# Performance work log

Measured on AMD Instinct MI355X. Metric: run time of the kernel, lower is better.

Reference implementation:

```python
import jax, jax.numpy as jnp
import numpy as np
from jax import lax

B, H, S = 256, 256, 512


def setup_inputs() -> dict:
    key = jax.random.key(0)
    ks = jax.random.split(key, 7)
    sc = 1.0 / np.sqrt(H).astype(np.float32)
    tree_state = jax.random.normal(ks[0], (B, H), jnp.float32)
    seq_states = jax.random.normal(ks[1], (B, H, S), jnp.float32)
    seq_mask = jax.random.randint(ks[2], (B, S), 0, 2, jnp.int32)
    W_ih = jax.random.uniform(ks[3], (3 * H, H), jnp.float32, -sc, sc)
    W_hh = jax.random.uniform(ks[4], (3 * H, H), jnp.float32, -sc, sc)
    b_ih = jax.random.uniform(ks[5], (3 * H,), jnp.float32, -sc, sc)
    b_hh = jax.random.uniform(ks[6], (3 * H,), jnp.float32, -sc, sc)
    return {"tree_state": tree_state, "seq_states": seq_states, "seq_mask": seq_mask,
            "W_ih": W_ih, "W_hh": W_hh, "b_ih": b_ih, "b_hh": b_hh}


def _gru_cell(x, h, W_ih, W_hh, b_ih, b_hh):
    # torch.nn.GRUCell math. x, h: (B, H); W_*: (3H, H); b_*: (3H,)
    gi = x @ W_ih.T + b_ih          # (B, 3H)
    gh = h @ W_hh.T + b_hh          # (B, 3H)
    i_r, i_z, i_n = jnp.split(gi, 3, axis=-1)
    h_r, h_z, h_n = jnp.split(gh, 3, axis=-1)
    r = jax.nn.sigmoid(i_r + h_r)
    z = jax.nn.sigmoid(i_z + h_z)
    n = jnp.tanh(i_n + r * h_n)
    return (1.0 - z) * n + z * h


def reference(tree_state, seq_states, seq_mask, W_ih, W_hh, b_ih, b_hh):
    # sequential recurrent scan over the seq axis of seq_states (batch, hid, seq)
    xs = jnp.transpose(seq_states, (2, 0, 1))  # (S, B, H)

    def step(h, x):
        h_new = _gru_cell(x, h, W_ih, W_hh, b_ih, b_hh)
        return h_new, h_new

    _, outs = lax.scan(step, tree_state, xs)      # (S, B, H)
    rnn_out = jnp.transpose(outs, (1, 0, 2))      # (B, S, H)
    # get_final_encoder_states: last unmasked timestep per row
    last_idx = jnp.maximum(jnp.sum(seq_mask, axis=1) - 1, 0)  # (B,)
    final = jnp.take_along_axis(rnn_out, last_idx[:, None, None], axis=1)  # (B,1,H)
    return final[:, 0, :]
```

## Files before the change

### kernel.cpp

```cpp
#include <hip/hip_runtime.h>
#include <hip/hip_bf16.h>

#define HH 256
#define SSL 512
#define G3 768

using short8 = __attribute__((ext_vector_type(8))) short;
using f32x4  = __attribute__((ext_vector_type(4))) float;

__device__ __forceinline__ unsigned short f2bf(float f) {
  unsigned int u = __float_as_uint(f);
  u += 0x7FFFu + ((u >> 16) & 1u);
  return (unsigned short)(u >> 16);
}
__device__ __forceinline__ float bf2f(unsigned short b) {
  return __uint_as_float(((unsigned int)b) << 16);
}
__device__ __forceinline__ void sync_step() {
  asm volatile("s_waitcnt lgkmcnt(0)" ::: "memory");
  __builtin_amdgcn_s_barrier();
  __builtin_amdgcn_sched_barrier(0);
}

__global__ __launch_bounds__(256) void prep_pack(
    const float* __restrict__ Wih, const float* __restrict__ Whh,
    unsigned short* __restrict__ wih_bf, unsigned short* __restrict__ whh_frag)
{
  int blk = blockIdx.x;
  if (blk < 96) {
    int base = (blk * 256 + threadIdx.x) * 4;
#pragma unroll
    for (int i = 0; i < 4; i++) {
      int u = base + i;
      float a = Wih[2 * u], b = Wih[2 * u + 1];
      ((unsigned int*)wih_bf)[u] = (unsigned int)f2bf(a) | ((unsigned int)f2bf(b) << 16);
    }
  } else {
    int gid = (blk - 96) * 256 + threadIdx.x;
    int f = gid >> 6, l = gid & 63;
    int kt = f & 7, mt = (f >> 3) & 3, g = (f >> 5) % 3, w = f / 96;
    int row = g * HH + w * 64 + mt * 16 + (l & 15);
    int k0  = kt * 32 + (l >> 4) * 8;
    const float* src = Whh + (size_t)row * HH + k0;
    unsigned int o[4];
#pragma unroll
    for (int i = 0; i < 4; i++)
      o[i] = (unsigned int)f2bf(src[2 * i]) | ((unsigned int)f2bf(src[2 * i + 1]) << 16);
    *(uint4*)(whh_frag + ((size_t)f * 64 + l) * 8) = *(uint4*)o;
  }
}

__global__ __launch_bounds__(512, 2) void gi_gemm(
    const float* __restrict__ X, const unsigned short* __restrict__ Wb,
    const float* __restrict__ bih, const float* __restrict__ bhh,
    unsigned short* __restrict__ gi)
{
  __shared__ __align__(16) unsigned short Al[128 * 256];
  __shared__ __align__(16) unsigned short Bl[128 * 256];
  __shared__ __align__(16) unsigned short Dl[64][136];
  __shared__ float biasl[G3];

  const int tid  = threadIdx.x;
  const int lane = tid & 63;
  const int wave = tid >> 6;
  const int wm   = wave >> 2;
  const int wn   = wave & 3;
  const int n16  = lane & 15;
  const int quad = lane >> 4;

  const int mblk = blockIdx.x;
  const int b    = mblk >> 2;
  const int s0   = (mblk & 3) * 128;

  const float* Xb = X + (size_t)b * (HH * SSL);

  for (int i = tid; i < G3; i += 512)
    biasl[i] = bih[i] + (i < 2 * HH ? bhh[i] : 0.f);

  float4 xs[4][2][2];
#pragma unroll
  for (int kt = 0; kt < 4; kt++)
#pragma unroll
    for (int q = 0; q < 2; q++) {
      int idx = tid + 512 * q, sq = idx & 31, a = idx >> 5;
      const float* p = Xb + (size_t)(kt * 64 + 2 * a) * SSL + s0 + 4 * sq;
      xs[kt][q][0] = *(const float4*)p;
      xs[kt][q][1] = *(const float4*)(p + SSL);
    }
#pragma unroll
  for (int kt = 0; kt < 4; kt++)
#pragma unroll
    for (int q = 0; q < 2; q++) {
      int idx = tid + 512 * q, sq = idx & 31, a = idx >> 5;
      int c = a >> 2, d = a & 3;
#pragma unroll
      for (int r = 0; r < 4; r++) {
        int s = 4 * sq + r;
        int sw = (s + (s >> 3)) & 7;
        unsigned int u =
            (unsigned int)f2bf(((const float*)&xs[kt][q][0])[r]) |
            ((unsigned int)f2bf(((const float*)&xs[kt][q][1])[r]) << 16);
        *(unsigned int*)(Al + s * 256 + kt * 64 + ((c ^ sw) * 8) + d * 2) = u;
      }
    }

  {
    uint4 wv[8];
#pragma unroll
    for (int p = 0; p < 8; p++) {
      int cid = tid + 512 * p, j = cid >> 5, c = cid & 31;
      wv[p] = *(const uint4*)(Wb + (size_t)(0 * 128 + j) * HH + c * 8);
    }
#pragma unroll
    for (int p = 0; p < 8; p++) {
      int cid = tid + 512 * p, j = cid >> 5, c = cid & 31;
      int sw = (j + (j >> 3)) & 7;
      *(uint4*)(Bl + j * 256 + (c >> 3) * 64 + (((c & 7) ^ sw) * 8)) = wv[p];
    }
  }
  __syncthreads();

  short8 af[4][8];
#pragma unroll
  for (int mt = 0; mt < 4; mt++) {
    int s = wm * 64 + mt * 16 + n16;
    int sw = (s + (s >> 3)) & 7;
#pragma unroll
    for (int kkk = 0; kkk < 8; kkk++) {
      int kt = kkk >> 1, c3 = (kkk & 1) * 4 + quad;
      af[mt][kkk] = *(const short8*)(Al + s * 256 + kt * 64 + ((c3 ^ sw) * 8));
    }
  }

  for (int jb = 0; jb < 6; jb++) {
    float bb0 = biasl[jb * 128 + wn * 32 + 0 * 16 + n16];
    float bb1 = biasl[jb * 128 + wn * 32 + 1 * 16 + n16];

    f32x4 acc[4][2];
#pragma unroll
    for (int mt = 0; mt < 4; mt++)
#pragma unroll
      for (int nt = 0; nt < 2; nt++) acc[mt][nt] = f32x4{0.f, 0.f, 0.f, 0.f};

#pragma unroll
    for (int kkk = 0; kkk < 8; kkk++) {
      short8 bfr[2];
      int kt = kkk >> 1, c3 = (kkk & 1) * 4 + quad;
#pragma unroll
      for (int nt = 0; nt < 2; nt++) {
        int j = wn * 32 + nt * 16 + n16;
        int sw = (j + (j >> 3)) & 7;
        bfr[nt] = *(const short8*)(Bl + j * 256 + kt * 64 + ((c3 ^ sw) * 8));
      }
#pragma unroll
      for (int mt = 0; mt < 4; mt++)
#pragma unroll
        for (int nt = 0; nt < 2; nt++)
          acc[mt][nt] = __builtin_amdgcn_mfma_f32_16x16x32_bf16(af[mt][kkk], bfr[nt], acc[mt][nt], 0, 0, 0);
    }
    __syncthreads();

#pragma unroll
    for (int c = 0; c < 2; c++) {
      if (wm == c) {
#pragma unroll
        for (int mt = 0; mt < 4; mt++)
#pragma unroll
          for (int nt = 0; nt < 2; nt++) {
            float bb = nt ? bb1 : bb0;
#pragma unroll
            for (int r = 0; r < 4; r++)
              Dl[mt * 16 + quad * 4 + r][wn * 32 + nt * 16 + n16] =
                  f2bf(acc[mt][nt][r] + bb);
          }
      }
      __syncthreads();
      {
        int row = tid >> 3, seg = tid & 7;
        short8 v0 = *(const short8*)&Dl[row][seg * 16];
        short8 v1 = *(const short8*)&Dl[row][seg * 16 + 8];
        size_t go = ((size_t)(b * SSL + s0 + c * 64 + row)) * G3 + jb * 128 + seg * 16;
        *(short8*)(gi + go) = v0;
        *(short8*)(gi + go + 8) = v1;
      }
      __syncthreads();
    }

    if (jb < 5) {
      uint4 wv[8];
#pragma unroll
      for (int p = 0; p < 8; p++) {
        int cid = tid + 512 * p, j = cid >> 5, c = cid & 31;
        wv[p] = *(const uint4*)(Wb + (size_t)((jb + 1) * 128 + j) * HH + c * 8);
      }
#pragma unroll
      for (int p = 0; p < 8; p++) {
        int cid = tid + 512 * p, j = cid >> 5, c = cid & 31;
        int sw = (j + (j >> 3)) & 7;
        *(uint4*)(Bl + j * 256 + (c >> 3) * 64 + (((c & 7) ^ sw) * 8)) = wv[p];
      }
      __syncthreads();
    }
  }
}

__global__ __launch_bounds__(256, 1) void gru_scan(
    const float* __restrict__ tree, const int* __restrict__ mask,
    const unsigned short* __restrict__ wfrag, const float* __restrict__ bhh,
    const unsigned short* __restrict__ gi, float* __restrict__ out)
{
  __shared__ __align__(16) unsigned short hbuf[2][1088];
  __shared__ int lsum[4];

  const int tid  = threadIdx.x;
  const int lane = tid & 63;
  const int w    = tid >> 6;
  const int n16  = lane & 15;
  const int quad = lane >> 4;
  const int b    = n16 & 3;
  const int rep  = n16 >> 2;
  const int brow0 = blockIdx.x * 4;
  const int jbase = w * 64 + rep * 16 + quad * 4;

  if (tid < 4) lsum[tid] = 0;

  f32x4 h4 = *(const f32x4*)(tree + (size_t)(brow0 + b) * HH + jbase);

  const int wslot = ((w * 2 + (rep >> 1)) * 17 + b * 4 + ((rep & 1) * 2 + (quad >> 1))) * 8
                  + (quad & 1) * 4;
  {
    unsigned long long u =
        (unsigned long long)((unsigned)f2bf(h4[0]) | ((unsigned)f2bf(h4[1]) << 16)) |
        ((unsigned long long)((unsigned)f2bf(h4[2]) | ((unsigned)f2bf(h4[3]) << 16)) << 32);
    *(unsigned long long*)&hbuf[0][wslot] = u;
  }
  {
    const int* mp = mask + (size_t)(brow0 + w) * SSL + lane * 8;
    int4 a = *(const int4*)mp;
    int4 c = *(const int4*)(mp + 4);
    atomicAdd(&lsum[w], a.x + a.y + a.z + a.w + c.x + c.y + c.z + c.w);
  }

  short8 awA[2][4][8];
  short8 awV[4][8];
#pragma unroll
  for (int g = 0; g < 2; g++)
#pragma unroll
    for (int mt = 0; mt < 4; mt++)
#pragma unroll
      for (int kt = 0; kt < 8; kt++) {
        int F = ((w * 3 + g) * 4 + mt) * 8 + kt;
        awA[g][mt][kt] = *(const short8*)(wfrag + ((size_t)F * 64 + lane) * 8);
      }
#pragma unroll
  for (int mt = 0; mt < 4; mt++)
#pragma unroll
    for (int kt = 0; kt < 8; kt++) {
      int F = ((w * 3 + 2) * 4 + mt) * 8 + kt;
      awV[mt][kt] = *(const short8*)(wfrag + ((size_t)F * 64 + lane) * 8);
    }
#pragma unroll
  for (int g = 0; g < 2; g++)
#pragma unroll
    for (int mt = 0; mt < 4; mt++)
#pragma unroll
      for (int kt = 0; kt < 8; kt++)
        asm volatile("" : "+a"(awA[g][mt][kt]));
#pragma unroll
  for (int mt = 0; mt < 4; mt++)
#pragma unroll
    for (int kt = 0; kt < 8; kt++)
      asm volatile("" : "+v"(awV[mt][kt]));

  f32x4 bh4 = *(const f32x4*)(bhh + 2 * HH + jbase);

  const unsigned short* gip = gi + (size_t)(brow0 + b) * SSL * G3 + jbase;
  unsigned long long gA[3], gB[3];
#pragma unroll
  for (int g = 0; g < 3; g++) gA[g] = *(const unsigned long long*)(gip + (size_t)0 * G3 + g * HH);
#pragma unroll
  for (int g = 0; g < 3; g++) gB[g] = *(const unsigned long long*)(gip + (size_t)1 * G3 + g * HH);

  __syncthreads();
  int mylast = lsum[b] - 1; if (mylast < 0) mylast = 0;

  auto step = [&](int t, unsigned long long* gv) {
    const int cb = t & 1, nb = cb ^ 1;
    unsigned long long g0 = gv[0], g1 = gv[1], g2 = gv[2];

    const unsigned short* hp = &hbuf[cb][0] + ((n16 & 3) * 4 + quad) * 8;
    short8 hb[8];
#pragma unroll
    for (int kt = 0; kt < 8; kt++)
      hb[kt] = *(const short8*)(hp + kt * (17 * 8));

    int tn = (t + 2 < SSL) ? t + 2 : SSL - 1;
    gv[0] = *(const unsigned long long*)(gip + (size_t)tn * G3 + 0 * HH);
    gv[1] = *(const unsigned long long*)(gip + (size_t)tn * G3 + 1 * HH);
    gv[2] = *(const unsigned long long*)(gip + (size_t)tn * G3 + 2 * HH);

    f32x4 selR, selZ, selN;
#pragma unroll
    for (int mp = 0; mp < 2; mp++) {
      const int m0 = 2 * mp, m1 = 2 * mp + 1;
      f32x4 ar0 = f32x4{0.f, 0.f, 0.f, 0.f}, az0 = ar0, an0 = ar0;
      f32x4 ar1 = ar0, az1 = ar0, an1 = ar0;
#pragma unroll
      for (int kt = 0; kt < 8; kt++) {
        ar0 = __builtin_amdgcn_mfma_f32_16x16x32_bf16(awA[0][m0][kt], hb[kt], ar0, 0, 0, 0);
        ar1 = __builtin_amdgcn_mfma_f32_16x16x32_bf16(awA[0][m1][kt], hb[kt], ar1, 0, 0, 0);
        az0 = __builtin_amdgcn_mfma_f32_16x16x32_bf16(awA[1][m0][kt], hb[kt], az0, 0, 0, 0);
        az1 = __builtin_amdgcn_mfma_f32_16x16x32_bf16(awA[1][m1][kt], hb[kt], az1, 0, 0, 0);
        an0 = __builtin_amdgcn_mfma_f32_16x16x32_bf16(awV[m0][kt],    hb[kt], an0, 0, 0, 0);
        an1 = __builtin_amdgcn_mfma_f32_16x16x32_bf16(awV[m1][kt],    hb[kt], an1, 0, 0, 0);
      }
      if (mp == 0) {
        selR = (rep == 0) ? ar0 : ar1;
        selZ = (rep == 0) ? az0 : az1;
        selN = (rep == 0) ? an0 : an1;
      } else {
        selR = (rep == 2) ? ar0 : ((rep == 3) ? ar1 : selR);
        selZ = (rep == 2) ? az0 : ((rep == 3) ? az1 : selZ);
        selN = (rep == 2) ? an0 : ((rep == 3) ? an1 : selN);
      }
    }

#pragma unroll
    for (int e = 0; e < 4; e++) {
      float gr = bf2f((unsigned short)((g0 >> (16 * e)) & 0xFFFFull));
      float gz = bf2f((unsigned short)((g1 >> (16 * e)) & 0xFFFFull));
      float gn = bf2f((unsigned short)((g2 >> (16 * e)) & 0xFFFFull));
      float r = __builtin_amdgcn_rcpf(1.f + __expf(-(selR[e] + gr)));
      float z = __builtin_amdgcn_rcpf(1.f + __expf(-(selZ[e] + gz)));
      float a = gn + r * (selN[e] + bh4[e]);
      float nn = 1.f - 2.f * __builtin_amdgcn_rcpf(__expf(2.f * a) + 1.f);
      h4[e] = nn + z * (h4[e] - nn);
    }
    {
      unsigned long long u =
          (unsigned long long)((unsigned)f2bf(h4[0]) | ((unsigned)f2bf(h4[1]) << 16)) |
          ((unsigned long long)((unsigned)f2bf(h4[2]) | ((unsigned)f2bf(h4[3]) << 16)) << 32);
      *(unsigned long long*)&hbuf[nb][wslot] = u;
    }
    if (t == mylast) {
      *(f32x4*)(out + (size_t)(brow0 + b) * HH + jbase) = h4;
    }
    sync_step();
  };

  for (int t = 0; t < SSL; t += 2) {
    step(t, gA);
    step(t + 1, gB);
  }
}

extern "C" void kernel_launch(void* const* d_in, const int* in_sizes, int n_in,
                              void* d_out, int out_size, void* d_ws, size_t ws_size,
                              hipStream_t stream) {
  const float* tree = (const float*)d_in[0];
  const float* seq  = (const float*)d_in[1];
  const int*   mask = (const int*)d_in[2];
  const float* Wih  = (const float*)d_in[3];
  const float* Whh  = (const float*)d_in[4];
  const float* bih  = (const float*)d_in[5];
  const float* bhh  = (const float*)d_in[6];
  float* out = (float*)d_out;

  unsigned short* gi      = (unsigned short*)d_ws;
  unsigned short* wih_bf  = (unsigned short*)((char*)d_ws + 201326592);
  unsigned short* whh_frag= (unsigned short*)((char*)d_ws + 201719808);

  prep_pack<<<192, 256, 0, stream>>>(Wih, Whh, wih_bf, whh_frag);
  gi_gemm<<<1024, 512, 0, stream>>>(seq, wih_bf, bih, bhh, gi);
  gru_scan<<<64, 256, 0, stream>>>(tree, mask, whh_frag, bhh, gi, out);
}
```

Before: 874.2 us.

## Spill part of recurrent weights to LDS and widen MFMA chains in GRU scan

In the scan kernel the last two k-tiles of the n-gate weights now live in LDS instead of registers, freeing VGPRs so all twelve accumulators can be kept live and the MFMA chains interleaved across four m-tiles. The LDS weight fragments are reloaded every timestep. In the prep kernel the next weight tile's global load is issued before the MFMA loop so it overlaps compute, and the output write loop is unrolled manually. The per-step LDS reads add traffic on the serial critical path, and more live accumulators raise register pressure.

Result: slower. 1.078 ms (+23.3%).

```diff
diff --git a/kernel.cpp b/kernel.cpp
--- a/kernel.cpp
+++ b/kernel.cpp
@@ -105,17 +105,17 @@
     }
 
   {
-    uint4 wv[8];
+    uint4 wv0[8];
 #pragma unroll
     for (int p = 0; p < 8; p++) {
       int cid = tid + 512 * p, j = cid >> 5, c = cid & 31;
-      wv[p] = *(const uint4*)(Wb + (size_t)(0 * 128 + j) * HH + c * 8);
+      wv0[p] = *(const uint4*)(Wb + (size_t)(0 * 128 + j) * HH + c * 8);
     }
 #pragma unroll
     for (int p = 0; p < 8; p++) {
       int cid = tid + 512 * p, j = cid >> 5, c = cid & 31;
       int sw = (j + (j >> 3)) & 7;
-      *(uint4*)(Bl + j * 256 + (c >> 3) * 64 + (((c & 7) ^ sw) * 8)) = wv[p];
+      *(uint4*)(Bl + j * 256 + (c >> 3) * 64 + (((c & 7) ^ sw) * 8)) = wv0[p];
     }
   }
   __syncthreads();
@@ -135,6 +135,15 @@
   for (int jb = 0; jb < 6; jb++) {
     float bb0 = biasl[jb * 128 + wn * 32 + 0 * 16 + n16];
     float bb1 = biasl[jb * 128 + wn * 32 + 1 * 16 + n16];
+
+    uint4 wv[8];
+    if (jb < 5) {
+#pragma unroll
+      for (int p = 0; p < 8; p++) {
+        int cid = tid + 512 * p, j = cid >> 5, c = cid & 31;
+        wv[p] = *(const uint4*)(Wb + (size_t)((jb + 1) * 128 + j) * HH + c * 8);
+      }
+    }
 
     f32x4 acc[4][2];
 #pragma unroll
@@ -160,39 +169,51 @@
     }
     __syncthreads();
 
-#pragma unroll
-    for (int c = 0; c < 2; c++) {
-      if (wm == c) {
-#pragma unroll
-        for (int mt = 0; mt < 4; mt++)
-#pragma unroll
-          for (int nt = 0; nt < 2; nt++) {
-            float bb = nt ? bb1 : bb0;
-#pragma unroll
-            for (int r = 0; r < 4; r++)
-              Dl[mt * 16 + quad * 4 + r][wn * 32 + nt * 16 + n16] =
-                  f2bf(acc[mt][nt][r] + bb);
-          }
-      }
-      __syncthreads();
-      {
-        int row = tid >> 3, seg = tid & 7;
-        short8 v0 = *(const short8*)&Dl[row][seg * 16];
-        short8 v1 = *(const short8*)&Dl[row][seg * 16 + 8];
-        size_t go = ((size_t)(b * SSL + s0 + c * 64 + row)) * G3 + jb * 128 + seg * 16;
-        *(short8*)(gi + go) = v0;
-        *(short8*)(gi + go + 8) = v1;
-      }
-      __syncthreads();
+    if (wm == 0) {
+#pragma unroll
+      for (int mt = 0; mt < 4; mt++)
+#pragma unroll
+        for (int nt = 0; nt < 2; nt++) {
+          float bb = nt ? bb1 : bb0;
+#pragma unroll
+          for (int r = 0; r < 4; r++)
+            Dl[mt * 16 + quad * 4 + r][wn * 32 + nt * 16 + n16] =
+                f2bf(acc[mt][nt][r] + bb);
+        }
+    }
+    __syncthreads();
+    {
+      int row = tid >> 3, seg = tid & 7;
+      short8 v0 = *(const short8*)&Dl[row][seg * 16];
+      short8 v1 = *(const short8*)&Dl[row][seg * 16 + 8];
+      size_t go = ((size_t)(b * SSL + s0 + row)) * G3 + jb * 128 + seg * 16;
+      *(short8*)(gi + go) = v0;
+      *(short8*)(gi + go + 8) = v1;
+    }
+    __syncthreads();
+    if (wm == 1) {
+#pragma unroll
+      for (int mt = 0; mt < 4; mt++)
+#pragma unroll
+        for (int nt = 0; nt < 2; nt++) {
+          float bb = nt ? bb1 : bb0;
+#pragma unroll
+          for (int r = 0; r < 4; r++)
+            Dl[mt * 16 + quad * 4 + r][wn * 32 + nt * 16 + n16] =
+                f2bf(acc[mt][nt][r] + bb);
+        }
+    }
+    __syncthreads();
+    {
+      int row = tid >> 3, seg = tid & 7;
+      short8 v0 = *(const short8*)&Dl[row][seg * 16];
+      short8 v1 = *(const short8*)&Dl[row][seg * 16 + 8];
+      size_t go = ((size_t)(b * SSL + s0 + 64 + row)) * G3 + jb * 128 + seg * 16;
+      *(short8*)(gi + go) = v0;
+      *(short8*)(gi + go + 8) = v1;
     }
 
     if (jb < 5) {
-      uint4 wv[8];
-#pragma unroll
-      for (int p = 0; p < 8; p++) {
-        int cid = tid + 512 * p, j = cid >> 5, c = cid & 31;
-        wv[p] = *(const uint4*)(Wb + (size_t)((jb + 1) * 128 + j) * HH + c * 8);
-      }
 #pragma unroll
       for (int p = 0; p < 8; p++) {
         int cid = tid + 512 * p, j = cid >> 5, c = cid & 31;
@@ -209,6 +230,7 @@
     const unsigned short* __restrict__ wfrag, const float* __restrict__ bhh,
     const unsigned short* __restrict__ gi, float* __restrict__ out)
 {
+  __shared__ __align__(16) unsigned short wlds[32 * 512];
   __shared__ __align__(16) unsigned short hbuf[2][1088];
   __shared__ int lsum[4];
 
@@ -224,6 +246,16 @@
 
   if (tid < 4) lsum[tid] = 0;
 
+#pragma unroll
+  for (int i = 0; i < 8; i++) {
+    int cid = tid + 256 * i;
+    int l = cid & 63, f = cid >> 6;
+    int wp = f >> 3, mt = (f >> 1) & 3, k = f & 1;
+    int F = ((wp * 3 + 2) * 4 + mt) * 8 + 6 + k;
+    *(uint4*)(wlds + ((size_t)f * 64 + l) * 8) =
+        *(const uint4*)(wfrag + ((size_t)F * 64 + l) * 8);
+  }
+
   f32x4 h4 = *(const f32x4*)(tree + (size_t)(brow0 + b) * HH + jbase);
 
   const int wslot = ((w * 2 + (rep >> 1)) * 17 + b * 4 + ((rep & 1) * 2 + (quad >> 1))) * 8
@@ -242,7 +274,7 @@
   }
 
   short8 awA[2][4][8];
-  short8 awV[4][8];
+  short8 awV[4][6];
 #pragma unroll
   for (int g = 0; g < 2; g++)
 #pragma unroll
@@ -255,7 +287,7 @@
 #pragma unroll
   for (int mt = 0; mt < 4; mt++)
 #pragma unroll
-    for (int kt = 0; kt < 8; kt++) {
+    for (int kt = 0; kt < 6; kt++) {
       int F = ((w * 3 + 2) * 4 + mt) * 8 + kt;
       awV[mt][kt] = *(const short8*)(wfrag + ((size_t)F * 64 + lane) * 8);
     }
@@ -269,7 +301,7 @@
 #pragma unroll
   for (int mt = 0; mt < 4; mt++)
 #pragma unroll
-    for (int kt = 0; kt < 8; kt++)
+    for (int kt = 0; kt < 6; kt++)
       asm volatile("" : "+v"(awV[mt][kt]));
 
   f32x4 bh4 = *(const f32x4*)(bhh + 2 * HH + jbase);
@@ -299,31 +331,42 @@
     gv[1] = *(const unsigned long long*)(gip + (size_t)tn * G3 + 1 * HH);
     gv[2] = *(const unsigned long long*)(gip + (size_t)tn * G3 + 2 * HH);
 
-    f32x4 selR, selZ, selN;
-#pragma unroll
-    for (int mp = 0; mp < 2; mp++) {
-      const int m0 = 2 * mp, m1 = 2 * mp + 1;
-      f32x4 ar0 = f32x4{0.f, 0.f, 0.f, 0.f}, az0 = ar0, an0 = ar0;
-      f32x4 ar1 = ar0, az1 = ar0, an1 = ar0;
-#pragma unroll
-      for (int kt = 0; kt < 8; kt++) {
-        ar0 = __builtin_amdgcn_mfma_f32_16x16x32_bf16(awA[0][m0][kt], hb[kt], ar0, 0, 0, 0);
-        ar1 = __builtin_amdgcn_mfma_f32_16x16x32_bf16(awA[0][m1][kt], hb[kt], ar1, 0, 0, 0);
-        az0 = __builtin_amdgcn_mfma_f32_16x16x32_bf16(awA[1][m0][kt], hb[kt], az0, 0, 0, 0);
-        az1 = __builtin_amdgcn_mfma_f32_16x16x32_bf16(awA[1][m1][kt], hb[kt], az1, 0, 0, 0);
-        an0 = __builtin_amdgcn_mfma_f32_16x16x32_bf16(awV[m0][kt],    hb[kt], an0, 0, 0, 0);
-        an1 = __builtin_amdgcn_mfma_f32_16x16x32_bf16(awV[m1][kt],    hb[kt], an1, 0, 0, 0);
-      }
-      if (mp == 0) {
-        selR = (rep == 0) ? ar0 : ar1;
-        selZ = (rep == 0) ? az0 : az1;
-        selN = (rep == 0) ? an0 : an1;
-      } else {
-        selR = (rep == 2) ? ar0 : ((rep == 3) ? ar1 : selR);
-        selZ = (rep == 2) ? az0 : ((rep == 3) ? az1 : selZ);
-        selN = (rep == 2) ? an0 : ((rep == 3) ? an1 : selN);
-      }
-    }
+    f32x4 accr[4], accz[4], accn[4];
+#pragma unroll
+    for (int m = 0; m < 4; m++) {
+      accr[m] = f32x4{0.f, 0.f, 0.f, 0.f};
+      accz[m] = f32x4{0.f, 0.f, 0.f, 0.f};
+      accn[m] = f32x4{0.f, 0.f, 0.f, 0.f};
+    }
+    short8 w2a[4], w2b[4];
+#pragma unroll
+    for (int kt = 0; kt < 8; kt++) {
+      if (kt == 4) {
+#pragma unroll
+        for (int m = 0; m < 4; m++)
+          w2a[m] = *(const short8*)(wlds + ((size_t)(((w * 4 + m) * 2 + 0)) * 64 + lane) * 8);
+      }
+      if (kt == 6) {
+#pragma unroll
+        for (int m = 0; m < 4; m++)
+          w2b[m] = *(const short8*)(wlds + ((size_t)(((w * 4 + m) * 2 + 1)) * 64 + lane) * 8);
+      }
+#pragma unroll
+      for (int m = 0; m < 4; m++)
+        accr[m] = __builtin_amdgcn_mfma_f32_16x16x32_bf16(awA[0][m][kt], hb[kt], accr[m], 0, 0, 0);
+#pragma unroll
+      for (int m = 0; m < 4; m++)
+        accz[m] = __builtin_amdgcn_mfma_f32_16x16x32_bf16(awA[1][m][kt], hb[kt], accz[m], 0, 0, 0);
+#pragma unroll
+      for (int m = 0; m < 4; m++) {
+        short8 wn = (kt < 6) ? awV[m][kt] : ((kt == 6) ? w2a[m] : w2b[m]);
+        accn[m] = __builtin_amdgcn_mfma_f32_16x16x32_bf16(wn, hb[kt], accn[m], 0, 0, 0);
+      }
+    }
+
+    f32x4 selR = (rep == 0) ? accr[0] : (rep == 1) ? accr[1] : (rep == 2) ? accr[2] : accr[3];
+    f32x4 selZ = (rep == 0) ? accz[0] : (rep == 1) ? accz[1] : (rep == 2) ? accz[2] : accz[3];
+    f32x4 selN = (rep == 0) ? accn[0] : (rep == 1) ? accn[1] : (rep == 2) ? accn[2] : accn[3];
 
 #pragma unroll
     for (int e = 0; e < 4; e++) {
```

## Pre-swizzle W_ih and stream it into LDS via global_load_lds, drop LDS epilogue

Applied to the files above, without the earlier changes.

The prep kernel now writes W_ih in bf16 already in the swizzled LDS layout. gi_gemm then loads each weight block directly global→LDS with global_load_lds instead of going through registers and ds_write. The next block's weight load is issued before the output epilogue, and the LDS-staged coalesced store of gi is replaced by direct per-element 2-byte global stores. This removes several barriers and register staging, at the cost of scattered narrow global writes for the gate-input output.

Result: no change. 861.3 us (-1.5%).

```diff
diff --git a/kernel.cpp b/kernel.cpp
--- a/kernel.cpp
+++ b/kernel.cpp
@@ -4,6 +4,9 @@
 #define HH 256
 #define SSL 512
 #define G3 768
+
+#define AS1 __attribute__((address_space(1)))
+#define AS3 __attribute__((address_space(3)))
 
 using short8 = __attribute__((ext_vector_type(8))) short;
 using f32x4  = __attribute__((ext_vector_type(4))) float;
@@ -28,13 +31,19 @@
 {
   int blk = blockIdx.x;
   if (blk < 96) {
-    int base = (blk * 256 + threadIdx.x) * 4;
-#pragma unroll
-    for (int i = 0; i < 4; i++) {
-      int u = base + i;
-      float a = Wih[2 * u], b = Wih[2 * u + 1];
-      ((unsigned int*)wih_bf)[u] = (unsigned int)f2bf(a) | ((unsigned int)f2bf(b) << 16);
-    }
+    int chunk = blk * 256 + threadIdx.x;
+    int jb = chunk >> 12;
+    int rem = chunk & 4095;
+    int j = rem >> 5;
+    int c = rem & 31;
+    const float* src = Wih + (size_t)(jb * 128 + j) * HH + c * 8;
+    unsigned int o[4];
+#pragma unroll
+    for (int i = 0; i < 4; i++)
+      o[i] = (unsigned int)f2bf(src[2 * i]) | ((unsigned int)f2bf(src[2 * i + 1]) << 16);
+    int sw = (j + (j >> 3)) & 7;
+    size_t dst = (size_t)jb * 4096 + j * 32 + (c >> 3) * 8 + ((c & 7) ^ sw);
+    *(uint4*)(wih_bf + dst * 8) = *(uint4*)o;
   } else {
     int gid = (blk - 96) * 256 + threadIdx.x;
     int f = gid >> 6, l = gid & 63;
@@ -57,7 +66,6 @@
 {
   __shared__ __align__(16) unsigned short Al[128 * 256];
   __shared__ __align__(16) unsigned short Bl[128 * 256];
-  __shared__ __align__(16) unsigned short Dl[64][136];
   __shared__ float biasl[G3];
 
   const int tid  = threadIdx.x;
@@ -88,6 +96,14 @@
       xs[kt][q][1] = *(const float4*)(p + SSL);
     }
 #pragma unroll
+  for (int i = 0; i < 8; i++) {
+    int cid = wave * 8 + i;
+    const unsigned short* src = Wb + ((size_t)(0 * 4096 + cid * 64 + lane)) * 8;
+    __builtin_amdgcn_global_load_lds((const AS1 unsigned int*)src,
+                                     (AS3 unsigned int*)(Bl + (size_t)cid * 512),
+                                     16, 0, 0);
+  }
+#pragma unroll
   for (int kt = 0; kt < 4; kt++)
 #pragma unroll
     for (int q = 0; q < 2; q++) {
@@ -103,21 +119,6 @@
         *(unsigned int*)(Al + s * 256 + kt * 64 + ((c ^ sw) * 8) + d * 2) = u;
       }
     }
-
-  {
-    uint4 wv[8];
-#pragma unroll
-    for (int p = 0; p < 8; p++) {
-      int cid = tid + 512 * p, j = cid >> 5, c = cid & 31;
-      wv[p] = *(const uint4*)(Wb + (size_t)(0 * 128 + j) * HH + c * 8);
-    }
-#pragma unroll
-    for (int p = 0; p < 8; p++) {
-      int cid = tid + 512 * p, j = cid >> 5, c = cid & 31;
-      int sw = (j + (j >> 3)) & 7;
-      *(uint4*)(Bl + j * 256 + (c >> 3) * 64 + (((c & 7) ^ sw) * 8)) = wv[p];
-    }
-  }
   __syncthreads();
 
   short8 af[4][8];
@@ -160,47 +161,31 @@
     }
     __syncthreads();
 
-#pragma unroll
-    for (int c = 0; c < 2; c++) {
-      if (wm == c) {
-#pragma unroll
-        for (int mt = 0; mt < 4; mt++)
-#pragma unroll
-          for (int nt = 0; nt < 2; nt++) {
-            float bb = nt ? bb1 : bb0;
-#pragma unroll
-            for (int r = 0; r < 4; r++)
-              Dl[mt * 16 + quad * 4 + r][wn * 32 + nt * 16 + n16] =
-                  f2bf(acc[mt][nt][r] + bb);
-          }
-      }
-      __syncthreads();
-      {
-        int row = tid >> 3, seg = tid & 7;
-        short8 v0 = *(const short8*)&Dl[row][seg * 16];
-        short8 v1 = *(const short8*)&Dl[row][seg * 16 + 8];
-        size_t go = ((size_t)(b * SSL + s0 + c * 64 + row)) * G3 + jb * 128 + seg * 16;
-        *(short8*)(gi + go) = v0;
-        *(short8*)(gi + go + 8) = v1;
-      }
-      __syncthreads();
-    }
-
     if (jb < 5) {
-      uint4 wv[8];
-#pragma unroll
-      for (int p = 0; p < 8; p++) {
-        int cid = tid + 512 * p, j = cid >> 5, c = cid & 31;
-        wv[p] = *(const uint4*)(Wb + (size_t)((jb + 1) * 128 + j) * HH + c * 8);
-      }
-#pragma unroll
-      for (int p = 0; p < 8; p++) {
-        int cid = tid + 512 * p, j = cid >> 5, c = cid & 31;
-        int sw = (j + (j >> 3)) & 7;
-        *(uint4*)(Bl + j * 256 + (c >> 3) * 64 + (((c & 7) ^ sw) * 8)) = wv[p];
-      }
-      __syncthreads();
-    }
+#pragma unroll
+      for (int i = 0; i < 8; i++) {
+        int cid = wave * 8 + i;
+        const unsigned short* src = Wb + ((size_t)((jb + 1) * 4096 + cid * 64 + lane)) * 8;
+        __builtin_amdgcn_global_load_lds((const AS1 unsigned int*)src,
+                                         (AS3 unsigned int*)(Bl + (size_t)cid * 512),
+                                         16, 0, 0);
+      }
+    }
+
+#pragma unroll
+    for (int mt = 0; mt < 4; mt++)
+#pragma unroll
+      for (int nt = 0; nt < 2; nt++) {
+        float bb = nt ? bb1 : bb0;
+#pragma unroll
+        for (int r = 0; r < 4; r++) {
+          int row = s0 + wm * 64 + mt * 16 + quad * 4 + r;
+          size_t go = ((size_t)b * SSL + row) * G3 + jb * 128 + wn * 32 + nt * 16 + n16;
+          gi[go] = f2bf(acc[mt][nt][r] + bb);
+        }
+      }
+
+    if (jb < 5) __syncthreads();
   }
 }
 
```
